# Kernel optimization log

Measured on AMD Instinct MI355X. Metric: run time of the kernel, lower is better.

Reference implementation:

```python
import jax, jax.numpy as jnp
import numpy as np

B, S, D, H = 4, 2048, 1024, 16
HD = D // H  # head_dim = 64


def setup_inputs() -> dict:
    key = jax.random.key(0)
    ks = jax.random.split(key, 6)
    scale = 0.02
    x = jax.random.normal(ks[0], (B, S, D), dtype=jnp.float32)
    # per-head projection weights, torch Linear is y = x @ W.T; store as [H, D, HD]
    Wq = jax.random.normal(ks[1], (H, D, HD), dtype=jnp.float32) * scale
    Wk = jax.random.normal(ks[2], (H, D, HD), dtype=jnp.float32) * scale
    Wv = jax.random.normal(ks[3], (H, D, HD), dtype=jnp.float32) * scale
    Wo = jax.random.normal(ks[4], (D, D), dtype=jnp.float32) * scale  # torch [out, in]
    bo = jax.random.normal(ks[5], (D,), dtype=jnp.float32) * scale
    return {"x": x, "Wq": Wq, "Wk": Wk, "Wv": Wv, "Wo": Wo, "bo": bo}


def reference(x, Wq, Wk, Wv, Wo, bo):
    # project: [B,S,D] x [H,D,HD] -> [B,H,S,HD]
    q = jnp.einsum("bsd,hde->bhse", x, Wq)
    k = jnp.einsum("bsd,hde->bhse", x, Wk)
    v = jnp.einsum("bsd,hde->bhse", x, Wv)
    scores = jnp.einsum("bhse,bhte->bhst", q, k) / jnp.sqrt(jnp.float32(HD))
    causal = jnp.tril(jnp.ones((S, S), dtype=bool))  # same as registered tril mask
    scores = jnp.where(causal, scores, -jnp.inf)
    w = jax.nn.softmax(scores, axis=-1)
    out = jnp.einsum("bhst,bhte->bhse", w, v)  # [B,H,S,HD]
    # concat heads along feature dim: [B,S,H*HD] = [B,S,D]
    out = out.transpose(0, 2, 1, 3).reshape(B, S, D)
    # output projection: torch Linear y = x @ W.T + b
    return jnp.einsum("bsd,od->bso", out, Wo) + bo
```

## Files before the change

kernel.cpp:

```cpp
#include <hip/hip_runtime.h>
#include <hip/hip_bf16.h>

typedef __bf16 bf16x8 __attribute__((ext_vector_type(8)));
typedef float f32x4 __attribute__((ext_vector_type(4)));
typedef unsigned short u16x4 __attribute__((ext_vector_type(4)));
typedef unsigned short u16x8 __attribute__((ext_vector_type(8)));
typedef unsigned uint4v __attribute__((ext_vector_type(4)));

#define B_ 4
#define S_ 2048
#define D_ 1024
#define H_ 16
#define HD_ 64

__device__ __forceinline__ unsigned short f2bf(float f) {
  unsigned u = __float_as_uint(f);
  u += 0x7fff + ((u >> 16) & 1);
  return (unsigned short)(u >> 16);
}

__device__ __forceinline__ void gload16(const void* g, void* l) {
  __builtin_amdgcn_global_load_lds((const __attribute__((address_space(1))) unsigned int*)g,
                                   (__attribute__((address_space(3))) unsigned int*)l,
                                   16, 0, 0);
}

__global__ void pack_x_k(const float* __restrict__ in, unsigned short* __restrict__ out, int n4) {
  int i = blockIdx.x * blockDim.x + threadIdx.x;
  int stride = gridDim.x * blockDim.x;
  for (; i < n4; i += stride) {
    float4 v = reinterpret_cast<const float4*>(in)[i];
    u16x4 o = {f2bf(v.x), f2bf(v.y), f2bf(v.z), f2bf(v.w)};
    reinterpret_cast<u16x4*>(out)[i] = o;
  }
}

__global__ void pack_wqkv_k(const float* __restrict__ Wq, const float* __restrict__ Wk,
                            const float* __restrict__ Wv, unsigned short* __restrict__ Wt) {
  int o = blockIdx.x * blockDim.x + threadIdx.x;
  int n = o >> 10;
  int d = o & 1023;
  const float* W = (n < 1024) ? Wq : (n < 2048) ? Wk : Wv;
  int nn = n & 1023;
  int h = nn >> 6, e = nn & 63;
  Wt[o] = f2bf(W[(h << 16) + (d << 6) + e]);
}

__global__ __launch_bounds__(512, 2) void gemm256_k(const unsigned short* __restrict__ A,
                                                    const unsigned short* __restrict__ Bt,
                                                    unsigned short* __restrict__ QK,
                                                    unsigned short* __restrict__ VT,
                                                    int M, int N, int K) {
  __shared__ __align__(16) unsigned short lA0[2][128 * 64];
  __shared__ __align__(16) unsigned short lA1[2][128 * 64];
  __shared__ __align__(16) unsigned short lB[2][192 * 64];
  const int tid = threadIdx.x;
  const int wid = tid >> 6, lane = tid & 63;
  const int r = lane & 15, g = lane >> 4;
  const int wm = wid >> 2, wn = wid & 3;

  const int i_hw = blockIdx.y * gridDim.x + blockIdx.x;
  const int xcd = i_hw & 7, j = i_hw >> 3;
  const long arow0 = (long)((xcd & 3) * 8 + (j & 7)) * 256;
  const long bcol0 = (long)((xcd >> 2) * 8 + (j >> 3)) * 192;

  const f32x4 z4 = {0.f, 0.f, 0.f, 0.f};
  f32x4 acc[8][3];
#pragma unroll
  for (int m = 0; m < 8; ++m)
#pragma unroll
    for (int n = 0; n < 3; ++n) acc[m][n] = z4;

  auto stage_half = [&](int kt, int which) {
    const unsigned short* src = (which == 2) ? Bt + bcol0 * K : A + (arow0 + 128 * which) * K;
    const int k0 = kt << 6;
    unsigned short* base = (which == 0) ? &lA0[kt & 1][0]
                         : (which == 1) ? &lA1[kt & 1][0] : &lB[kt & 1][0];
    const int nch = (which == 2) ? 3 : 2;
    for (int c = 0; c < nch; ++c) {
      const int jj = c * 512 + tid;
      const int row = jj >> 3, cc = jj & 7;
      const int ccs = cc ^ (row & 7);
      gload16(src + (long)row * K + k0 + ccs * 8, base + jj * 8);
    }
  };

  bf16x8 af[4][2], bv[3][2];
  auto read_a = [&](const unsigned short* lbase) {
#pragma unroll
    for (int i2 = 0; i2 < 4; ++i2)
#pragma unroll
      for (int kk = 0; kk < 2; ++kk) {
        const int rowh = (2 * i2 + wm) * 16 + r;
        af[i2][kk] = *(const bf16x8*)&lbase[rowh * 64 + (((kk << 2) + g) ^ (rowh & 7)) * 8];
      }
  };
  auto read_b = [&](int buf) {
#pragma unroll
    for (int j2 = 0; j2 < 3; ++j2)
#pragma unroll
      for (int kk = 0; kk < 2; ++kk) {
        const int rowh = (4 * j2 + wn) * 16 + r;
        bv[j2][kk] = *(const bf16x8*)&lB[buf][rowh * 64 + (((kk << 2) + g) ^ (rowh & 7)) * 8];
      }
  };
  auto mma_h = [&](int mh) {
    __builtin_amdgcn_s_setprio(1);
#pragma unroll
    for (int kk = 0; kk < 2; ++kk)
#pragma unroll
      for (int i2 = 0; i2 < 4; ++i2)
#pragma unroll
        for (int j2 = 0; j2 < 3; ++j2)
          acc[4 * mh + i2][j2] = __builtin_amdgcn_mfma_f32_16x16x32_bf16(
              af[i2][kk], bv[j2][kk], acc[4 * mh + i2][j2], 0, 0, 0);
    __builtin_amdgcn_s_setprio(0);
  };

  const int nk = K >> 6;
  stage_half(0, 0);
  stage_half(0, 2);
  stage_half(0, 1);
  asm volatile("s_waitcnt vmcnt(2)" ::: "memory");
  asm volatile("s_barrier" ::: "memory");

  for (int t = 0; t < nk; ++t) {
    const int buf = t & 1;
    const bool pre = (t + 1 < nk);
    read_a(&lA0[buf][0]);
    read_b(buf);
    if (pre) { stage_half(t + 1, 0); stage_half(t + 1, 2); }
    asm volatile("s_barrier" ::: "memory");
    mma_h(0);
    if (pre) asm volatile("s_waitcnt vmcnt(5)" ::: "memory");
    else     asm volatile("s_waitcnt vmcnt(0)" ::: "memory");
    asm volatile("s_waitcnt lgkmcnt(0)\n\ts_barrier" ::: "memory");
    read_a(&lA1[buf][0]);
    if (pre) stage_half(t + 1, 1);
    asm volatile("s_barrier" ::: "memory");
    mma_h(1);
    if (pre) asm volatile("s_waitcnt vmcnt(2)" ::: "memory");
    asm volatile("s_waitcnt lgkmcnt(0)\n\ts_barrier" ::: "memory");
  }

#pragma unroll
  for (int j2 = 0; j2 < 3; ++j2) {
    const long colb = bcol0 + (4 * j2 + wn) * 16;
    if (colb < 2048) {
#pragma unroll
      for (int m = 0; m < 8; ++m)
#pragma unroll
        for (int rr = 0; rr < 4; ++rr) {
          const long row = arow0 + (2 * m + wm) * 16 + g * 4 + rr;
          QK[row * 2048 + colb + r] = f2bf(acc[m][j2][rr]);
        }
    } else {
      const long vcol = colb - 2048 + r;
      const long h = vcol >> 6, e = vcol & 63;
#pragma unroll
      for (int m = 0; m < 8; ++m) {
        const long row0 = arow0 + (2 * m + wm) * 16 + g * 4;
        const long b = row0 >> 11, s = row0 & 2047;
        u16x4 w4;
#pragma unroll
        for (int rr = 0; rr < 4; ++rr) w4[rr] = f2bf(acc[m][j2][rr]);
        *(u16x4*)&VT[(((b << 4) + h) * 64 + e) * 2048 + s] = w4;
      }
    }
  }
}

__global__ __launch_bounds__(512, 2) void gemm_op_k(const unsigned short* __restrict__ A,
                                                    const unsigned short* __restrict__ Bt,
                                                    float* __restrict__ C,
                                                    const float* __restrict__ bias,
                                                    int M, int N, int K) {
  __shared__ __align__(16) unsigned short lA0[2][128 * 64];
  __shared__ __align__(16) unsigned short lA1[2][128 * 64];
  __shared__ __align__(16) unsigned short lB[2][128 * 64];
  const int tid = threadIdx.x;
  const int wid = tid >> 6, lane = tid & 63;
  const int r = lane & 15, g = lane >> 4;
  const int wm = wid >> 2, wn = wid & 3;

  const int i_hw = blockIdx.y * gridDim.x + blockIdx.x;
  const int xcd = i_hw & 7, j = i_hw >> 3;
  const long arow0 = (long)((xcd & 3) * 8 + (j & 7)) * 256;
  const long bcol0 = (long)((xcd >> 2) * 4 + (j >> 3)) * 128;

  const f32x4 z4 = {0.f, 0.f, 0.f, 0.f};
  f32x4 acc[8][2];
#pragma unroll
  for (int m = 0; m < 8; ++m)
#pragma unroll
    for (int n = 0; n < 2; ++n) acc[m][n] = z4;

  auto stage_half = [&](int kt, int which) {
    const unsigned short* src = (which == 2) ? Bt + bcol0 * K : A + (arow0 + 128 * which) * K;
    const int k0 = kt << 6;
    unsigned short* base = (which == 0) ? &lA0[kt & 1][0]
                         : (which == 1) ? &lA1[kt & 1][0] : &lB[kt & 1][0];
#pragma unroll
    for (int c = 0; c < 2; ++c) {
      const int jj = c * 512 + tid;
      const int row = jj >> 3, cc = jj & 7;
      const int ccs = cc ^ (row & 7);
      gload16(src + (long)row * K + k0 + ccs * 8, base + jj * 8);
    }
  };

  bf16x8 af[4][2], bv[2][2];
  auto read_a = [&](const unsigned short* lbase) {
#pragma unroll
    for (int i2 = 0; i2 < 4; ++i2)
#pragma unroll
      for (int kk = 0; kk < 2; ++kk) {
        const int rowh = (2 * i2 + wm) * 16 + r;
        af[i2][kk] = *(const bf16x8*)&lbase[rowh * 64 + (((kk << 2) + g) ^ (rowh & 7)) * 8];
      }
  };
  auto read_b = [&](int buf) {
#pragma unroll
    for (int j2 = 0; j2 < 2; ++j2)
#pragma unroll
      for (int kk = 0; kk < 2; ++kk) {
        const int rowh = (4 * j2 + wn) * 16 + r;
        bv[j2][kk] = *(const bf16x8*)&lB[buf][rowh * 64 + (((kk << 2) + g) ^ (rowh & 7)) * 8];
      }
  };
  auto mma_h = [&](int mh) {
    __builtin_amdgcn_s_setprio(1);
#pragma unroll
    for (int kk = 0; kk < 2; ++kk)
#pragma unroll
      for (int i2 = 0; i2 < 4; ++i2)
#pragma unroll
        for (int j2 = 0; j2 < 2; ++j2)
          acc[4 * mh + i2][j2] = __builtin_amdgcn_mfma_f32_16x16x32_bf16(
              af[i2][kk], bv[j2][kk], acc[4 * mh + i2][j2], 0, 0, 0);
    __builtin_amdgcn_s_setprio(0);
  };

  const int nk = K >> 6;
  stage_half(0, 0);
  stage_half(0, 2);
  stage_half(0, 1);
  asm volatile("s_waitcnt vmcnt(2)" ::: "memory");
  asm volatile("s_barrier" ::: "memory");

  for (int t = 0; t < nk; ++t) {
    const int buf = t & 1;
    const bool pre = (t + 1 < nk);
    read_a(&lA0[buf][0]);
    read_b(buf);
    if (pre) { stage_half(t + 1, 0); stage_half(t + 1, 2); }
    asm volatile("s_barrier" ::: "memory");
    mma_h(0);
    if (pre) asm volatile("s_waitcnt vmcnt(4)" ::: "memory");
    else     asm volatile("s_waitcnt vmcnt(0)" ::: "memory");
    asm volatile("s_waitcnt lgkmcnt(0)\n\ts_barrier" ::: "memory");
    read_a(&lA1[buf][0]);
    if (pre) stage_half(t + 1, 1);
    asm volatile("s_barrier" ::: "memory");
    mma_h(1);
    if (pre) asm volatile("s_waitcnt vmcnt(2)" ::: "memory");
    asm volatile("s_waitcnt lgkmcnt(0)\n\ts_barrier" ::: "memory");
  }

#pragma unroll
  for (int m = 0; m < 8; ++m)
#pragma unroll
    for (int n = 0; n < 2; ++n)
#pragma unroll
      for (int rr = 0; rr < 4; ++rr) {
        const long row = arow0 + (2 * m + wm) * 16 + g * 4 + rr;
        const long col = bcol0 + (4 * n + wn) * 16 + r;
        C[row * N + col] = acc[m][n][rr] + bias[col];
      }
}

__global__ __launch_bounds__(256, 2) void attn_k(const unsigned short* __restrict__ qk,
                                                 const unsigned short* __restrict__ vt,
                                                 unsigned short* __restrict__ out) {
  __shared__ __align__(16) unsigned short lK[2][64 * 64];
  __shared__ __align__(16) unsigned short lVt[2][64 * 64];

  const int tid = threadIdx.x, wid = tid >> 6, lane = tid & 63;
  const int r = lane & 15, g = lane >> 4;
  const int bh = blockIdx.x;
  const int b = bh >> 4, h = bh & 15;
  const int qb = 31 - (int)blockIdx.y;
  const int q0 = qb * 64;

  const unsigned short* Qg = qk + ((long)b * S_) * 2048 + h * 64;
  const unsigned short* Kg = Qg + 1024;
  const unsigned short* Vg = vt + ((long)(b * 16 + h)) * 64 * 2048;

  const int qrow = q0 + wid * 16 + r;
  bf16x8 qf[2];
#pragma unroll
  for (int kk = 0; kk < 2; ++kk)
    qf[kk] = *(const bf16x8*)&Qg[(long)qrow * 2048 + kk * 32 + g * 8];

  const f32x4 z4 = {0.f, 0.f, 0.f, 0.f};
  f32x4 o[4];
#pragma unroll
  for (int nt = 0; nt < 4; ++nt) o[nt] = z4;
  float m_i = -1e30f;
  float l_i = 0.f;

  const int srow = tid >> 3, scc = tid & 7;
  const int sccs = (scc ^ (srow & 7)) << 3;
  const unsigned short* kp = Kg + (long)srow * 2048 + sccs;
  const unsigned short* kp2 = Kg + (long)(srow + 32) * 2048 + sccs;
  const unsigned short* vp = Vg + (long)srow * 2048 + sccs;
  const unsigned short* vp2 = Vg + (long)(srow + 32) * 2048 + sccs;
  auto stage = [&](int buf, long koff, long voff) {
    gload16(kp + koff, &lK[buf][tid * 8]);
    gload16(kp2 + koff, &lK[buf][(256 + tid) * 8]);
    gload16(vp + voff, &lVt[buf][tid * 8]);
    gload16(vp2 + voff, &lVt[buf][(256 + tid) * 8]);
  };

  const int ntiles = qb + 1;
  stage(0, 0, 0);

  for (int t = 0; t < ntiles; ++t) {
    const int cur = t & 1;
    __syncthreads();
    if (t + 1 < ntiles) stage(cur ^ 1, (long)(t + 1) * 64 * 2048, (long)(t + 1) * 64);

    const int t0 = t << 6;
    const bool diag = (t == ntiles - 1);

    f32x4 st[4];
#pragma unroll
    for (int tt = 0; tt < 4; ++tt) st[tt] = z4;
    __builtin_amdgcn_s_setprio(1);
#pragma unroll
    for (int kk = 0; kk < 2; ++kk)
#pragma unroll
      for (int tt = 0; tt < 4; ++tt) {
        const int row = tt * 16 + r, cc = kk * 4 + g;
        bf16x8 kf = *(const bf16x8*)&lK[cur][(row * 8 + (cc ^ (row & 7))) * 8];
        st[tt] = __builtin_amdgcn_mfma_f32_16x16x32_bf16(kf, qf[kk], st[tt], 0, 0, 0);
      }
    __builtin_amdgcn_s_setprio(0);

    float sv[16];
    if (diag) {
#pragma unroll
      for (int tt = 0; tt < 4; ++tt)
#pragma unroll
        for (int rg = 0; rg < 4; ++rg) {
          float s = st[tt][rg];
          if (t0 + tt * 16 + g * 4 + rg > qrow) s = -1e30f;
          sv[tt * 4 + rg] = s;
        }
    } else {
#pragma unroll
      for (int tt = 0; tt < 4; ++tt)
#pragma unroll
        for (int rg = 0; rg < 4; ++rg) sv[tt * 4 + rg] = st[tt][rg];
    }
    float h0 = fmaxf(fmaxf(fmaxf(sv[0], sv[1]), fmaxf(sv[2], sv[3])),
                     fmaxf(fmaxf(sv[4], sv[5]), fmaxf(sv[6], sv[7])));
    float h1 = fmaxf(fmaxf(fmaxf(sv[8], sv[9]), fmaxf(sv[10], sv[11])),
                     fmaxf(fmaxf(sv[12], sv[13]), fmaxf(sv[14], sv[15])));
    const float pmax = fmaxf(h0, h1);
    const bool defer = __all(pmax - m_i <= 64.f);
    float corr = 1.f;
    if (!defer) {
      float mx = fmaxf(pmax, m_i);
      mx = fmaxf(mx, __shfl_xor(mx, 16, 64));
      mx = fmaxf(mx, __shfl_xor(mx, 32, 64));
      corr = __expf((m_i - mx) * 0.125f);
      m_i = mx;
    }
    const float m8 = m_i * 0.125f;
    float p[16];
    float rs = 0.f;
#pragma unroll
    for (int i = 0; i < 16; ++i) {
      p[i] = __expf(__builtin_fmaf(sv[i], 0.125f, -m8));
      rs += p[i];
    }
    rs += __shfl_xor(rs, 16, 64);
    rs += __shfl_xor(rs, 32, 64);
    l_i = l_i * corr + rs;
    unsigned cw[4][2];
#pragma unroll
    for (int tt = 0; tt < 4; ++tt)
#pragma unroll
      for (int e = 0; e < 2; ++e)
        asm("v_cvt_pk_bf16_f32 %0, %1, %2"
            : "=v"(cw[tt][e]) : "v"(p[tt * 4 + 2 * e]), "v"(p[tt * 4 + 2 * e + 1]));
    bf16x8 pf[2];
#pragma unroll
    for (int kk = 0; kk < 2; ++kk) {
      unsigned x0 = cw[2 * kk][0], y0 = cw[2 * kk + 1][0];
      unsigned x1 = cw[2 * kk][1], y1 = cw[2 * kk + 1][1];
      asm volatile("v_permlane32_swap_b32 %0, %1" : "+v"(x0), "+v"(y0));
      asm volatile("v_permlane16_swap_b32 %0, %1" : "+v"(x0), "+v"(y0));
      asm volatile("v_permlane32_swap_b32 %0, %1" : "+v"(x1), "+v"(y1));
      asm volatile("v_permlane16_swap_b32 %0, %1" : "+v"(x1), "+v"(y1));
      uint4v w = {x0, x1, y0, y1};
      pf[kk] = *(bf16x8*)&w;
    }
    if (!defer) {
#pragma unroll
      for (int rr = 0; rr < 4; ++rr) {
        const float c = __shfl(corr, g * 4 + rr, 64);
#pragma unroll
        for (int nt = 0; nt < 4; ++nt) o[nt][rr] *= c;
      }
    }

    __builtin_amdgcn_s_setprio(1);
#pragma unroll
    for (int kk = 0; kk < 2; ++kk)
#pragma unroll
      for (int nt = 0; nt < 4; ++nt) {
        const int row = nt * 16 + r, cc = kk * 4 + g;
        const bf16x8 vf = *(const bf16x8*)&lVt[cur][(row * 8 + (cc ^ (row & 7))) * 8];
        o[nt] = __builtin_amdgcn_mfma_f32_16x16x32_bf16(pf[kk], vf, o[nt], 0, 0, 0);
      }
    __builtin_amdgcn_s_setprio(0);
  }

  float linv[4];
#pragma unroll
  for (int rr = 0; rr < 4; ++rr)
    linv[rr] = 1.f / __shfl(l_i, g * 4 + rr, 64);
#pragma unroll
  for (int nt = 0; nt < 4; ++nt)
#pragma unroll
    for (int rr = 0; rr < 4; ++rr) {
      const long s = q0 + wid * 16 + g * 4 + rr;
      out[((long)b * S_ + s) * 1024 + h * 64 + nt * 16 + r] = f2bf(o[nt][rr] * linv[rr]);
    }
}

extern "C" void kernel_launch(void* const* d_in, const int* in_sizes, int n_in,
                              void* d_out, int out_size, void* d_ws, size_t ws_size,
                              hipStream_t stream) {
  const float* x = (const float*)d_in[0];
  const float* Wq = (const float*)d_in[1];
  const float* Wk = (const float*)d_in[2];
  const float* Wv = (const float*)d_in[3];
  const float* Wo = (const float*)d_in[4];
  const float* bo = (const float*)d_in[5];
  float* out = (float*)d_out;

  char* ws = (char*)d_ws;
  unsigned short* Xb = (unsigned short*)(ws);
  unsigned short* Wt = (unsigned short*)(ws + (16ul << 20));
  unsigned short* Wob = (unsigned short*)(ws + (22ul << 20));
  unsigned short* QK = (unsigned short*)(ws + (24ul << 20));
  unsigned short* VT = (unsigned short*)(ws + (56ul << 20));
  unsigned short* AO = (unsigned short*)(ws + (72ul << 20));

  pack_x_k<<<2048, 256, 0, stream>>>(x, Xb, (B_ * S_ * D_) / 4);
  pack_x_k<<<512, 256, 0, stream>>>(Wo, Wob, (D_ * D_) / 4);
  pack_wqkv_k<<<(3 * D_ * D_) / 256, 256, 0, stream>>>(Wq, Wk, Wv, Wt);

  gemm256_k<<<dim3(32, 16), 512, 0, stream>>>(Xb, Wt, QK, VT, B_ * S_, 3 * D_, D_);
  attn_k<<<dim3(64, 32), 256, 0, stream>>>(QK, VT, AO);
  gemm_op_k<<<dim3(32, 8), 512, 0, stream>>>(AO, Wob, out, bo, B_ * S_, D_, D_);
}
```

Before: 175.2 us.

## Shrink QKV GEMM tile to 128x192 with simpler double-buffered pipeline

```diff
diff --git a/kernel.cpp b/kernel.cpp
--- a/kernel.cpp
+++ b/kernel.cpp
@@ -46,13 +46,12 @@
   Wt[o] = f2bf(W[(h << 16) + (d << 6) + e]);
 }
 
-__global__ __launch_bounds__(512, 2) void gemm256_k(const unsigned short* __restrict__ A,
+__global__ __launch_bounds__(512, 4) void gemm256_k(const unsigned short* __restrict__ A,
                                                     const unsigned short* __restrict__ Bt,
                                                     unsigned short* __restrict__ QK,
                                                     unsigned short* __restrict__ VT,
                                                     int M, int N, int K) {
-  __shared__ __align__(16) unsigned short lA0[2][128 * 64];
-  __shared__ __align__(16) unsigned short lA1[2][128 * 64];
+  __shared__ __align__(16) unsigned short lA[2][128 * 64];
   __shared__ __align__(16) unsigned short lB[2][192 * 64];
   const int tid = threadIdx.x;
   const int wid = tid >> 6, lane = tid & 63;
@@ -61,41 +60,50 @@
 
   const int i_hw = blockIdx.y * gridDim.x + blockIdx.x;
   const int xcd = i_hw & 7, j = i_hw >> 3;
-  const long arow0 = (long)((xcd & 3) * 8 + (j & 7)) * 256;
-  const long bcol0 = (long)((xcd >> 2) * 8 + (j >> 3)) * 192;
+  const long arow0 = (long)((xcd & 3) * 16 + (j & 15)) * 128;
+  const long bcol0 = (long)((xcd >> 2) * 8 + (j >> 4)) * 192;
 
   const f32x4 z4 = {0.f, 0.f, 0.f, 0.f};
-  f32x4 acc[8][3];
-#pragma unroll
-  for (int m = 0; m < 8; ++m)
+  f32x4 acc[4][3];
+#pragma unroll
+  for (int m = 0; m < 4; ++m)
 #pragma unroll
     for (int n = 0; n < 3; ++n) acc[m][n] = z4;
 
-  auto stage_half = [&](int kt, int which) {
-    const unsigned short* src = (which == 2) ? Bt + bcol0 * K : A + (arow0 + 128 * which) * K;
+  auto stage = [&](int kt) {
     const int k0 = kt << 6;
-    unsigned short* base = (which == 0) ? &lA0[kt & 1][0]
-                         : (which == 1) ? &lA1[kt & 1][0] : &lB[kt & 1][0];
-    const int nch = (which == 2) ? 3 : 2;
-    for (int c = 0; c < nch; ++c) {
+    const int buf = kt & 1;
+#pragma unroll
+    for (int c = 0; c < 2; ++c) {
       const int jj = c * 512 + tid;
       const int row = jj >> 3, cc = jj & 7;
       const int ccs = cc ^ (row & 7);
-      gload16(src + (long)row * K + k0 + ccs * 8, base + jj * 8);
-    }
-  };
-
-  bf16x8 af[4][2], bv[3][2];
-  auto read_a = [&](const unsigned short* lbase) {
+      gload16(A + (arow0 + row) * K + k0 + ccs * 8, &lA[buf][jj * 8]);
+    }
+#pragma unroll
+    for (int c = 0; c < 3; ++c) {
+      const int jj = c * 512 + tid;
+      const int row = jj >> 3, cc = jj & 7;
+      const int ccs = cc ^ (row & 7);
+      gload16(Bt + (bcol0 + row) * K + k0 + ccs * 8, &lB[buf][jj * 8]);
+    }
+  };
+
+  const int nk = K >> 6;
+  stage(0);
+  __syncthreads();
+
+  for (int t = 0; t < nk; ++t) {
+    const int buf = t & 1;
+    if (t + 1 < nk) stage(t + 1);
+    bf16x8 af[4][2], bv[3][2];
 #pragma unroll
     for (int i2 = 0; i2 < 4; ++i2)
 #pragma unroll
       for (int kk = 0; kk < 2; ++kk) {
         const int rowh = (2 * i2 + wm) * 16 + r;
-        af[i2][kk] = *(const bf16x8*)&lbase[rowh * 64 + (((kk << 2) + g) ^ (rowh & 7)) * 8];
-      }
-  };
-  auto read_b = [&](int buf) {
+        af[i2][kk] = *(const bf16x8*)&lA[buf][rowh * 64 + (((kk << 2) + g) ^ (rowh & 7)) * 8];
+      }
 #pragma unroll
     for (int j2 = 0; j2 < 3; ++j2)
 #pragma unroll
@@ -103,8 +111,6 @@
         const int rowh = (4 * j2 + wn) * 16 + r;
         bv[j2][kk] = *(const bf16x8*)&lB[buf][rowh * 64 + (((kk << 2) + g) ^ (rowh & 7)) * 8];
       }
-  };
-  auto mma_h = [&](int mh) {
     __builtin_amdgcn_s_setprio(1);
 #pragma unroll
     for (int kk = 0; kk < 2; ++kk)
@@ -112,35 +118,10 @@
       for (int i2 = 0; i2 < 4; ++i2)
 #pragma unroll
         for (int j2 = 0; j2 < 3; ++j2)
-          acc[4 * mh + i2][j2] = __builtin_amdgcn_mfma_f32_16x16x32_bf16(
-              af[i2][kk], bv[j2][kk], acc[4 * mh + i2][j2], 0, 0, 0);
+          acc[i2][j2] = __builtin_amdgcn_mfma_f32_16x16x32_bf16(
+              af[i2][kk], bv[j2][kk], acc[i2][j2], 0, 0, 0);
     __builtin_amdgcn_s_setprio(0);
-  };
-
-  const int nk = K >> 6;
-  stage_half(0, 0);
-  stage_half(0, 2);
-  stage_half(0, 1);
-  asm volatile("s_waitcnt vmcnt(2)" ::: "memory");
-  asm volatile("s_barrier" ::: "memory");
-
-  for (int t = 0; t < nk; ++t) {
-    const int buf = t & 1;
-    const bool pre = (t + 1 < nk);
-    read_a(&lA0[buf][0]);
-    read_b(buf);
-    if (pre) { stage_half(t + 1, 0); stage_half(t + 1, 2); }
-    asm volatile("s_barrier" ::: "memory");
-    mma_h(0);
-    if (pre) asm volatile("s_waitcnt vmcnt(5)" ::: "memory");
-    else     asm volatile("s_waitcnt vmcnt(0)" ::: "memory");
-    asm volatile("s_waitcnt lgkmcnt(0)\n\ts_barrier" ::: "memory");
-    read_a(&lA1[buf][0]);
-    if (pre) stage_half(t + 1, 1);
-    asm volatile("s_barrier" ::: "memory");
-    mma_h(1);
-    if (pre) asm volatile("s_waitcnt vmcnt(2)" ::: "memory");
-    asm volatile("s_waitcnt lgkmcnt(0)\n\ts_barrier" ::: "memory");
+    __syncthreads();
   }
 
 #pragma unroll
@@ -148,7 +129,7 @@
     const long colb = bcol0 + (4 * j2 + wn) * 16;
     if (colb < 2048) {
 #pragma unroll
-      for (int m = 0; m < 8; ++m)
+      for (int m = 0; m < 4; ++m)
 #pragma unroll
         for (int rr = 0; rr < 4; ++rr) {
           const long row = arow0 + (2 * m + wm) * 16 + g * 4 + rr;
@@ -158,7 +139,7 @@
       const long vcol = colb - 2048 + r;
       const long h = vcol >> 6, e = vcol & 63;
 #pragma unroll
-      for (int m = 0; m < 8; ++m) {
+      for (int m = 0; m < 4; ++m) {
         const long row0 = arow0 + (2 * m + wm) * 16 + g * 4;
         const long b = row0 >> 11, s = row0 & 2047;
         u16x4 w4;
@@ -464,7 +445,7 @@
   pack_x_k<<<512, 256, 0, stream>>>(Wo, Wob, (D_ * D_) / 4);
   pack_wqkv_k<<<(3 * D_ * D_) / 256, 256, 0, stream>>>(Wq, Wk, Wv, Wt);
 
-  gemm256_k<<<dim3(32, 16), 512, 0, stream>>>(Xb, Wt, QK, VT, B_ * S_, 3 * D_, D_);
+  gemm256_k<<<dim3(64, 16), 512, 0, stream>>>(Xb, Wt, QK, VT, B_ * S_, 3 * D_, D_);
   attn_k<<<dim3(64, 32), 256, 0, stream>>>(QK, VT, AO);
   gemm_op_k<<<dim3(32, 8), 512, 0, stream>>>(AO, Wob, out, bo, B_ * S_, D_, D_);
 }
```

Result: no change. 175.2 us (median of 2 runs) (+0.0%).
